# Optimization experiments

Measured on AMD Instinct MI355X. Metric: run time of the kernel, lower is better.

## Reference

```python
import jax, jax.numpy as jnp
import numpy as np

EPS = 1e-5
SLOPE = 0.2  # leakyrelu negative slope (gcn_lib default)
K = 9

def knn_idx(x, k):
    # x: (B, C, N) -> idx (B, N, k) of k nearest neighbors, self excluded
    B, C, N = x.shape
    xx = jnp.sum(x * x, axis=1)                       # (B, N)
    inner = jnp.einsum('bcn,bcm->bnm', x, x)          # (B, N, N)
    dist = xx[:, :, None] - 2.0 * inner + xx[:, None, :]
    dist = dist + jnp.eye(N, dtype=x.dtype) * 1e10    # mask self
    _, idx = jax.lax.top_k(-dist, k)                  # nearest = largest -dist
    return idx

def bn(h, g, b, axes):
    m = jnp.mean(h, axis=axes, keepdims=True)
    v = jnp.var(h, axis=axes, keepdims=True)
    sh = [1] * h.ndim; sh[1] = -1
    return (h - m) / jnp.sqrt(v + EPS) * g.reshape(sh) + b.reshape(sh)

def leaky(h):
    return jnp.where(h >= 0, h, SLOPE * h)

def edge_conv(x, idx, W, g, b):
    # x: (B, C, N); idx: (B, N, k); W: (O, 2C)
    B, C, N = x.shape
    k = idx.shape[-1]
    x_j = jax.vmap(lambda xb, ib: xb[:, ib])(x, idx)  # (B, C, N, k)
    x_i = jnp.broadcast_to(x[:, :, :, None], (B, C, N, k))
    edge = jnp.concatenate([x_i, x_j - x_i], axis=1)  # (B, 2C, N, k)
    h = jnp.einsum('oc,bcnk->bonk', W, edge)
    h = leaky(bn(h, g, b, (0, 2, 3)))
    return jnp.max(h, axis=-1)                        # (B, O, N)

def setup_inputs() -> dict:
    key = jax.random.key(0)
    ks = jax.random.split(key, 24)
    B, N = 8, 4096
    d = {}
    d['x'] = jax.random.normal(ks[0], (B, 3, N), dtype=jnp.float32)
    d['coords'] = jax.random.normal(ks[1], (B, 3, N), dtype=jnp.float32)
    def w(k_, o, i): return jax.random.normal(k_, (o, i), dtype=jnp.float32) * (2.0 / i) ** 0.5
    # edge conv layers (bias=False, batchnorm affine)
    d['w1'], d['g1'], d['b1'] = w(ks[2], 64, 6),    jnp.ones(64),  jnp.zeros(64)
    d['w2'], d['g2'], d['b2'] = w(ks[3], 64, 128),  jnp.ones(64),  jnp.zeros(64)
    d['w3'], d['g3'], d['b3'] = w(ks[4], 128, 128), jnp.ones(128), jnp.zeros(128)
    d['w4'], d['g4'], d['b4'] = w(ks[5], 256, 256), jnp.ones(256), jnp.zeros(256)
    # decoder fusion conv [512 -> 1024]
    d['wf'], d['bf'] = w(ks[6], 1024, 512), jnp.zeros(1024)
    d['gf'], d['betaf'] = jnp.ones(1024), jnp.zeros(1024)
    # classifier [2048 -> 512 -> 256 -> 40]
    d['wc1'], d['bc1'] = w(ks[7], 512, 2048), jnp.zeros(512)
    d['gc1'], d['betac1'] = jnp.ones(512), jnp.zeros(512)
    d['wc2'], d['bc2'] = w(ks[8], 256, 512), jnp.zeros(256)
    d['gc2'], d['betac2'] = jnp.ones(256), jnp.zeros(256)
    d['wc3'], d['bc3'] = w(ks[9], 40, 256), jnp.zeros(40)
    return d

def reference(x, coords, w1, g1, b1, w2, g2, b2, w3, g3, b3, w4, g4, b4,
              wf, bf, gf, betaf, wc1, bc1, gc1, betac1, wc2, bc2, gc2, betac2, wc3, bc3):
    out1 = edge_conv(x,    knn_idx(x, K),    w1, g1, b1)   # (B, 64, N)
    out2 = edge_conv(out1, knn_idx(out1, K), w2, g2, b2)   # (B, 64, N)
    out3 = edge_conv(out2, knn_idx(out2, K), w3, g3, b3)   # (B, 128, N)
    out4 = edge_conv(out3, knn_idx(out3, K), w4, g4, b4)   # (B, 256, N)
    feat = jnp.concatenate([out1, out2, out3, out4], axis=1)  # (B, 512, N)
    fusion = jnp.einsum('oc,bcn->bon', wf, feat) + bf[None, :, None]
    fusion = leaky(bn(fusion, gf, betaf, (0, 2)))           # (B, 1024, N)
    x1 = jnp.max(fusion, axis=-1)                           # adaptive max pool
    x2 = jnp.mean(fusion, axis=-1)                          # adaptive avg pool
    h = jnp.concatenate([x1, x2], axis=1)                   # (B, 2048)
    h = leaky(bn(h @ wc1.T + bc1, gc1, betac1, (0,)))       # dropout = identity (eval)
    h = leaky(bn(h @ wc2.T + bc2, gc2, betac2, (0,)))
    logits = h @ wc3.T + bc3                                # (B, 40)
    return logits
```

## Files before the change

### kernel.cpp

```cpp
#include <hip/hip_runtime.h>
#include <math.h>
#include <float.h>


#define LEAKY(y) ((y) >= 0.f ? (y) : 0.2f * (y))

using f32x16 = __attribute__((ext_vector_type(16))) float;
using bf16x8 = __attribute__((ext_vector_type(8))) __bf16;
using short8v = __attribute__((ext_vector_type(8))) short;

__device__ inline ushort f2bf(float x) {
  unsigned u = __float_as_uint(x);
  unsigned r = (u + 0x7fff + ((u >> 16) & 1)) >> 16;
  return (ushort)r;
}

template<int C>
__global__ void xx_kernel(const float* __restrict__ xin, long bstride, int N,
                          float* __restrict__ xxg) {
  int n = blockIdx.x * 256 + threadIdx.x;
  int b = blockIdx.y;
  if (n < N) {
    const float* xb = xin + (long)b * bstride;
    float s = 0.f;
    #pragma unroll
    for (int c = 0; c < C; ++c) { float t = xb[(long)c * N + n]; s += t * t; }
    xxg[(long)b * N + n] = s;
  }
}

template<int C, int KCc>
__global__ __launch_bounds__(256) void pack3_kernel(const float* __restrict__ xin, long bstride,
                                                    int N, const float* __restrict__ xxg,
                                                    ushort* __restrict__ packR,
                                                    ushort* __restrict__ packC,
                                                    float* __restrict__ xpm) {
  __shared__ float xt[C][32];
  const int tid = threadIdx.x;
  const int pb = blockIdx.x, b = blockIdx.y;
  for (int i = tid; i < C * 32; i += 256) {
    int c = i >> 5, j = i & 31;
    xt[c][j] = xin[(long)b * bstride + (long)c * N + pb * 32 + j];
  }
  __syncthreads();
  for (int i = tid; i < 32 * C; i += 256) {
    int pt = i / C, c = i % C;
    xpm[((long)b * N + pb * 32 + pt) * C + c] = xt[c][pt];
  }
  const int PB = N >> 5;
  for (int it = tid; it < KCc * 64; it += 256) {
    int kc = it >> 6, l = it & 63;
    int pt = l & 31;
    union { ushort u[8]; short8v v; } R, Cc;
    #pragma unroll
    for (int e = 0; e < 8; ++e) {
      int kp = kc * 16 + ((l >> 5) << 3) + e;
      ushort rv = 0, cv = 0;
      if (kp < 3 * C) {
        int s = kp / C, c = kp % C;
        float xv = xt[c][pt];
        ushort hi = f2bf(xv);
        float hif = __uint_as_float((unsigned)hi << 16);
        ushort mid = f2bf(xv - hif);
        rv = (s == 2) ? mid : hi;
        cv = (s == 1) ? mid : hi;
      } else if (kp == 3 * C) {
        float xxv = xxg[(long)b * N + pb * 32 + pt];
        cv = f2bf(xxv);
        rv = 0xBF00;
      } else if (kp == 3 * C + 1) {
        float xxv = xxg[(long)b * N + pb * 32 + pt];
        ushort hi = f2bf(xxv);
        float hif = __uint_as_float((unsigned)hi << 16);
        cv = f2bf(xxv - hif);
        rv = 0xBF00;
      }
      R.u[e] = rv; Cc.u[e] = cv;
    }
    long off = (((long)b * PB + pb) * KCc + kc) * 512 + l * 8;
    *reinterpret_cast<short8v*>(&packR[off]) = R.v;
    *reinterpret_cast<short8v*>(&packC[off]) = Cc.v;
  }
}

#define KNN_SCAN(SELF)                                            \
  _Pragma("unroll")                                               \
  for (int reg = 0; reg < 16; ++reg) {                            \
    int m_loc = (reg & 3) + 8 * (reg >> 2) + 4 * hf;              \
    float d = fmaf(-2.0f, acc[reg], xr);                          \
    d = fmaxf(d, 0.f);                                            \
    unsigned key = (__float_as_uint(d) & KEYMASK) |               \
                   (unsigned)((t << 5) | m_loc);                  \
    if (SELF && ((mb << 5) | m_loc) == n_glob) key = 0xFFFFFFFFu; \
    if (key < tk[9]) {                                            \
      unsigned kc = key;                                          \
      _Pragma("unroll")                                           \
      for (int s_ = 0; s_ < 10; ++s_) {                           \
        unsigned mn_ = min(kc, tk[s_]);                           \
        kc = max(kc, tk[s_]);                                     \
        tk[s_] = mn_;                                             \
      }                                                           \
    }                                                             \
  }

template<int KCc, int MINW, int Z>
__global__ __launch_bounds__(256, MINW) void knn_v5(const ushort* __restrict__ packR,
                                                    const ushort* __restrict__ packC,
                                                    const float* __restrict__ xxg,
                                                    int N, int* __restrict__ cand) {
  constexpr int SA_ELEMS = KCc * 512;
  constexpr int SA_BYTES = SA_ELEMS * 2;
  constexpr int POOL = (2 * SA_BYTES > 10240) ? 2 * SA_BYTES : 10240;
  __shared__ __align__(16) char smem[POOL];
  ushort* const sA0 = (ushort*)smem;
  ushort* const sA1 = (ushort*)(smem + SA_BYTES);

  const int tid = threadIdx.x;
  const int b = blockIdx.y, rowblk = blockIdx.x, z = blockIdx.z;
  const int w = tid >> 6, l = tid & 63;
  const int lane31 = l & 31, hf = l >> 5;
  const int PB = N >> 5;
  const int HALF = PB / Z;
  const unsigned IDXMASK = (unsigned)(HALF * 32 - 1);
  const unsigned KEYMASK = ~IDXMASK;
  const int myblk = rowblk * 4 + w;

  const ushort* rp = packR + (((long)b * PB + myblk) * (long)KCc) * 512 + l * 8;
  bf16x8 bfr[KCc];
  #pragma unroll
  for (int kc = 0; kc < KCc; ++kc)
    bfr[kc] = *reinterpret_cast<const bf16x8*>(rp + kc * 512);

  const ushort* srcb = packC + ((long)b * PB) * (long)SA_ELEMS;
  const int mb0 = z * HALF;

  {
    const ushort* src = srcb + (long)mb0 * SA_ELEMS;
    for (int i = tid * 8; i < SA_ELEMS; i += 2048)
      __builtin_amdgcn_global_load_lds(
          (const __attribute__((address_space(1))) void*)(src + i),
          (__attribute__((address_space(3))) void*)(sA0 + i), 16, 0, 0);
  }

  const int n_glob = rowblk * 128 + w * 32 + lane31;
  const float xr = xxg[(long)b * N + n_glob];

  unsigned tk[10];
  #pragma unroll
  for (int s = 0; s < 10; ++s) tk[s] = 0xFFFFFFFFu;

  __syncthreads();

  for (int t = 0; t < HALF; ++t) {
    const int mb = mb0 + t;
    const ushort* curA = (t & 1) ? sA1 : sA0;
    ushort* nxtA = (t & 1) ? sA0 : sA1;
    if (t + 1 < HALF) {
      const ushort* src = srcb + (long)(mb + 1) * SA_ELEMS;
      for (int i = tid * 8; i < SA_ELEMS; i += 2048)
        __builtin_amdgcn_global_load_lds(
            (const __attribute__((address_space(1))) void*)(src + i),
            (__attribute__((address_space(3))) void*)(nxtA + i), 16, 0, 0);
    }
    f32x16 acc = {};
    #pragma unroll
    for (int kc = 0; kc < KCc; ++kc) {
      bf16x8 af = *reinterpret_cast<const bf16x8*>(curA + kc * 512 + l * 8);
      acc = __builtin_amdgcn_mfma_f32_32x32x16_bf16(af, bfr[kc], acc, 0, 0, 0);
    }
    if (mb == myblk) {
      KNN_SCAN(true)
    } else {
      KNN_SCAN(false)
    }
    __syncthreads();
  }

  unsigned* mK = (unsigned*)smem;
  const int row = w * 32 + lane31;
  #pragma unroll
  for (int s = 0; s < 10; ++s)
    mK[row * 20 + hf * 10 + s] = tk[s];
  __syncthreads();
  if (tid < 128) {
    int p0 = 0, p1 = 0;
    const long ob = ((long)b * N + rowblk * 128 + tid) * (Z * 10) + z * 10;
    const int base_m = z * HALF * 32;
    for (int s = 0; s < 10; ++s) {
      unsigned k0 = mK[tid * 20 + p0];
      unsigned k1 = mK[tid * 20 + 10 + p1];
      bool t0 = k0 < k1;
      unsigned kk = t0 ? k0 : k1;
      cand[ob + s] = base_m + (int)(kk & IDXMASK);
      if (t0) ++p0; else ++p1;
    }
  }
}

template<int C, int P>
__global__ __launch_bounds__(320) void rerank_kernel(const float* __restrict__ xpm,
                                                     int N, const float* __restrict__ xxg,
                                                     const int* __restrict__ cand,
                                                     int* __restrict__ idx_out) {
  constexpr int ROWS = 320 / P;
  __shared__ float sq[ROWS][C];
  __shared__ float sd[ROWS][P + 1];
  __shared__ int   si[ROWS][P + 1];
  const int tid = threadIdx.x;
  const int b = blockIdx.y, n0 = blockIdx.x * ROWS;
  const float* xb = xpm + (long)b * N * C;
  for (int i = tid; i < ROWS * C; i += 320) {
    int r = i / C, c = i % C;
    sq[r][c] = xb[(long)(n0 + r) * C + c];
  }
  __syncthreads();
  const int r = tid / P, j = tid % P;
  const int n = n0 + r;
  const int m = cand[((long)b * N + n) * P + j];
  const float* cv = xb + (long)m * C;
  float dot = 0.f;
  if constexpr ((C & 3) == 0) {
    for (int c = 0; c < C; c += 4) {
      float4 v4 = *reinterpret_cast<const float4*>(cv + c);
      dot = fmaf(sq[r][c + 0], v4.x, dot);
      dot = fmaf(sq[r][c + 1], v4.y, dot);
      dot = fmaf(sq[r][c + 2], v4.z, dot);
      dot = fmaf(sq[r][c + 3], v4.w, dot);
    }
  } else {
    for (int c = 0; c < C; ++c) dot = fmaf(sq[r][c], cv[c], dot);
  }
  float d = (xxg[(long)b * N + n] - 2.0f * dot) + xxg[(long)b * N + m];
  if (m == n) d = 3.0e38f;
  sd[r][j] = d; si[r][j] = m;
  __syncthreads();
  int rank = 0;
  #pragma unroll
  for (int t = 0; t < P; ++t) {
    float dd = sd[r][t]; int ii = si[r][t];
    if (dd < d || (dd == d && ii < m)) rank++;
  }
  if (rank < 9) idx_out[((long)b * N + n) * 9 + rank] = m;
}

__global__ void prep_wt(const float* __restrict__ W, int Cin, int O,
                        float* __restrict__ At, float* __restrict__ W2t) {
  int i = blockIdx.x * 256 + threadIdx.x;
  if (i < O * Cin) {
    int o = i % O, c = i / O;
    float w1v = W[(long)o * 2 * Cin + c];
    float w2v = W[(long)o * 2 * Cin + Cin + c];
    At[(long)c * O + o]  = w1v - w2v;
    W2t[(long)c * O + o] = w2v;
  }
}

__global__ __launch_bounds__(256) void gemm_cn_no(const float* __restrict__ Wt,
                                                  int C, int O,
                                                  const float* __restrict__ in,
                                                  long in_bstride, int N,
                                                  float* __restrict__ out) {
  const int tid = threadIdx.x;
  const int n0 = blockIdx.x * 64, o0 = blockIdx.y * 64, b = blockIdx.z;
  __shared__ float wT[128][64];
  __shared__ float inT[128][64];
  for (int i = tid; i < C * 64; i += 256) {
    int c = i >> 6, j = i & 63;
    wT[c][j]  = Wt[(long)c * O + o0 + j];
    inT[c][j] = in[(long)b * in_bstride + (long)c * N + n0 + j];
  }
  __syncthreads();
  const int tr = tid >> 4, tc = tid & 15;
  float acc[4][4];
  #pragma unroll
  for (int i = 0; i < 4; ++i)
    #pragma unroll
    for (int j = 0; j < 4; ++j) acc[i][j] = 0.f;
  for (int c = 0; c < C; ++c) {
    float4 a4 = *reinterpret_cast<const float4*>(&wT[c][4 * tr]);
    float4 b4 = *reinterpret_cast<const float4*>(&inT[c][4 * tc]);
    float av[4] = {a4.x, a4.y, a4.z, a4.w};
    float bv[4] = {b4.x, b4.y, b4.z, b4.w};
    #pragma unroll
    for (int i = 0; i < 4; ++i)
      #pragma unroll
      for (int j = 0; j < 4; ++j) acc[i][j] = fmaf(av[i], bv[j], acc[i][j]);
  }
  #pragma unroll
  for (int j = 0; j < 4; ++j) {
    float4 st = make_float4(acc[0][j], acc[1][j], acc[2][j], acc[3][j]);
    *reinterpret_cast<float4*>(&out[((long)b * N + n0 + 4 * tc + j) * O + o0 + 4 * tr]) = st;
  }
}

__global__ __launch_bounds__(256) void edge_pass(const float* __restrict__ u,
                                                 const float* __restrict__ v,
                                                 const int* __restrict__ idx,
                                                 int O, int N,
                                                 float* __restrict__ hmax,
                                                 float* __restrict__ hmin,
                                                 double* __restrict__ S1,
                                                 double* __restrict__ S2) {
  const int tid = threadIdx.x;
  const int n0 = blockIdx.x * 64, o0 = blockIdx.y * 64, b = blockIdx.z;
  __shared__ int sidx[64][9];
  __shared__ float4 redA[4][16];
  __shared__ float4 redB[4][16];
  for (int i = tid; i < 576; i += 256)
    ((int*)sidx)[i] = idx[((long)b * N + n0) * 9 + i];
  __syncthreads();
  const int nl = tid >> 4, oq = tid & 15;
  const long base = (long)b * N;
  const int ocol = o0 + 4 * oq;
  float4 s1 = make_float4(0.f, 0.f, 0.f, 0.f);
  float4 s2 = make_float4(0.f, 0.f, 0.f, 0.f);
  for (int g = 0; g < 4; ++g) {
    const int n = g * 16 + nl;
    const float4 u4 = *reinterpret_cast<const float4*>(&u[(base + n0 + n) * O + ocol]);
    float4 mx = make_float4(-3.0e38f, -3.0e38f, -3.0e38f, -3.0e38f);
    float4 mn = make_float4(3.0e38f, 3.0e38f, 3.0e38f, 3.0e38f);
    #pragma unroll
    for (int k = 0; k < 9; ++k) {
      int m = sidx[n][k];
      const float4 v4 = *reinterpret_cast<const float4*>(&v[(base + m) * O + ocol]);
      float hx = u4.x + v4.x, hy = u4.y + v4.y, hz = u4.z + v4.z, hw = u4.w + v4.w;
      s1.x += hx; s1.y += hy; s1.z += hz; s1.w += hw;
      s2.x = fmaf(hx, hx, s2.x); s2.y = fmaf(hy, hy, s2.y);
      s2.z = fmaf(hz, hz, s2.z); s2.w = fmaf(hw, hw, s2.w);
      mx.x = fmaxf(mx.x, hx); mx.y = fmaxf(mx.y, hy); mx.z = fmaxf(mx.z, hz); mx.w = fmaxf(mx.w, hw);
      mn.x = fminf(mn.x, hx); mn.y = fminf(mn.y, hy); mn.z = fminf(mn.z, hz); mn.w = fminf(mn.w, hw);
    }
    *reinterpret_cast<float4*>(&hmax[(base + n0 + n) * O + ocol]) = mx;
    *reinterpret_cast<float4*>(&hmin[(base + n0 + n) * O + ocol]) = mn;
  }
  s1.x += __shfl_xor(s1.x, 16); s1.y += __shfl_xor(s1.y, 16);
  s1.z += __shfl_xor(s1.z, 16); s1.w += __shfl_xor(s1.w, 16);
  s2.x += __shfl_xor(s2.x, 16); s2.y += __shfl_xor(s2.y, 16);
  s2.z += __shfl_xor(s2.z, 16); s2.w += __shfl_xor(s2.w, 16);
  s1.x += __shfl_xor(s1.x, 32); s1.y += __shfl_xor(s1.y, 32);
  s1.z += __shfl_xor(s1.z, 32); s1.w += __shfl_xor(s1.w, 32);
  s2.x += __shfl_xor(s2.x, 32); s2.y += __shfl_xor(s2.y, 32);
  s2.z += __shfl_xor(s2.z, 32); s2.w += __shfl_xor(s2.w, 32);
  if ((tid & 48) == 0) { redA[tid >> 6][oq] = s1; redB[tid >> 6][oq] = s2; }
  __syncthreads();
  if (tid < 16) {
    float4 a = redA[0][tid], bb = redB[0][tid];
    #pragma unroll
    for (int ww = 1; ww < 4; ++ww) {
      float4 t1 = redA[ww][tid], t2 = redB[ww][tid];
      a.x += t1.x; a.y += t1.y; a.z += t1.z; a.w += t1.w;
      bb.x += t2.x; bb.y += t2.y; bb.z += t2.z; bb.w += t2.w;
    }
    int o = o0 + 4 * tid;
    atomicAdd(&S1[o + 0], (double)a.x);  atomicAdd(&S1[o + 1], (double)a.y);
    atomicAdd(&S1[o + 2], (double)a.z);  atomicAdd(&S1[o + 3], (double)a.w);
    atomicAdd(&S2[o + 0], (double)bb.x); atomicAdd(&S2[o + 1], (double)bb.y);
    atomicAdd(&S2[o + 2], (double)bb.z); atomicAdd(&S2[o + 3], (double)bb.w);
  }
}

__global__ void finalize_scale(const double* __restrict__ S1, const double* __restrict__ S2,
                               const float* __restrict__ g, const float* __restrict__ beta,
                               double invM, int O, float* __restrict__ scale,
                               float* __restrict__ shift) {
  int o = blockIdx.x * 256 + threadIdx.x;
  if (o < O) {
    double mean = S1[o] * invM;
    double var = S2[o] * invM - mean * mean;
    double sc = (double)g[o] / sqrt(var + 1e-5);
    scale[o] = (float)sc;
    shift[o] = (float)((double)beta[o] - mean * sc);
  }
}

__global__ __launch_bounds__(256) void edge_out(const float* __restrict__ hmax,
                                                const float* __restrict__ hmin,
                                                const float* __restrict__ scale,
                                                const float* __restrict__ shift,
                                                int O, int N,
                                                float* __restrict__ outp, long out_bstride) {
  const int tid = threadIdx.x;
  const int b = blockIdx.y, n0 = blockIdx.x * 64;
  __shared__ float yt[64][65];
  const int ol = tid & 63, nl = tid >> 6;
  const long base = (long)b * N;
  for (int oc = 0; oc < O; oc += 64) {
    float sc = scale[oc + ol], sh = shift[oc + ol];
    __syncthreads();
    for (int ng = 0; ng < 16; ++ng) {
      int n = ng * 4 + nl;
      long off = (base + n0 + n) * O + oc + ol;
      float hv = (sc >= 0.f) ? hmax[off] : hmin[off];
      float y = sc * hv + sh;
      yt[ol][n] = LEAKY(y);
    }
    __syncthreads();
    for (int rr = 0; rr < 16; ++rr) {
      int r = rr * 4 + nl;
      outp[(long)b * out_bstride + (long)(oc + r) * N + n0 + ol] = yt[r][ol];
    }
  }
}

__global__ __launch_bounds__(256) void pack3_wf(const float* __restrict__ wf,
                                                ushort* __restrict__ packW) {
  __shared__ float wt[32][129];
  const int po = blockIdx.x;
  const int tid = threadIdx.x;
  for (int c0 = 0; c0 < 512; c0 += 128) {
    __syncthreads();
    for (int i = tid; i < 32 * 128; i += 256) {
      int o = i >> 7, c = i & 127;
      wt[o][c] = wf[(long)(po * 32 + o) * 512 + c0 + c];
    }
    __syncthreads();
    #pragma unroll
    for (int s = 0; s < 3; ++s) {
      int kc0 = (s * 512 + c0) >> 4;
      for (int it = tid; it < 8 * 64; it += 256) {
        int kcl = it >> 6, l = it & 63;
        union { ushort u[8]; short8v v; } P;
        #pragma unroll
        for (int e = 0; e < 8; ++e) {
          int kp = (kc0 + kcl) * 16 + ((l >> 5) << 3) + e;
          int c = kp - s * 512 - c0;
          float xv = wt[l & 31][c];
          ushort hi = f2bf(xv);
          if (s == 1) {
            float hif = __uint_as_float((unsigned)hi << 16);
            P.u[e] = f2bf(xv - hif);
          } else P.u[e] = hi;
        }
        *reinterpret_cast<short8v*>(&packW[((long)po * 96 + kc0 + kcl) * 512 + l * 8]) = P.v;
      }
    }
  }
}

__global__ __launch_bounds__(256) void pack3_feat(const float* __restrict__ feat, int N,
                                                  ushort* __restrict__ packB) {
  __shared__ float xt[64][33];
  const int pb = blockIdx.x, b = blockIdx.y;
  const int tid = threadIdx.x;
  const int PB = N >> 5;
  for (int c0 = 0; c0 < 512; c0 += 64) {
    __syncthreads();
    for (int i = tid; i < 64 * 32; i += 256) {
      int c = i >> 5, j = i & 31;
      xt[c][j] = feat[((long)b * 512 + c0 + c) * N + pb * 32 + j];
    }
    __syncthreads();
    #pragma unroll
    for (int s = 0; s < 3; ++s) {
      int kc0 = (s * 512 + c0) >> 4;
      for (int it = tid; it < 4 * 64; it += 256) {
        int kcl = it >> 6, l = it & 63;
        union { ushort u[8]; short8v v; } P;
        #pragma unroll
        for (int e = 0; e < 8; ++e) {
          int kp = (kc0 + kcl) * 16 + ((l >> 5) << 3) + e;
          int c = kp - s * 512 - c0;
          float xv = xt[c][l & 31];
          ushort hi = f2bf(xv);
          if (s == 2) {
            float hif = __uint_as_float((unsigned)hi << 16);
            P.u[e] = f2bf(xv - hif);
          } else P.u[e] = hi;
        }
        *reinterpret_cast<short8v*>(
            &packB[(((long)b * PB + pb) * 96 + kc0 + kcl) * 512 + l * 8]) = P.v;
      }
    }
  }
}

#define FUS_EPI(ACC, Q)                                                          \
  _Pragma("unroll")                                                              \
  for (int reg = 0; reg < 16; ++reg) {                                           \
    int o = ((z * 16 + (Q) * 4 + w) << 5) + (reg & 3) + 8 * (reg >> 2) + 4 * hf; \
    float h = ACC[reg] + bfb[o];                                                 \
    hbf[((long)b * 1024 + o) * 4096 + (nt << 5) + lane31] = f2bf(h);             \
    float mx = h, mn = h;                                                        \
    _Pragma("unroll")                                                            \
    for (int off = 1; off < 32; off <<= 1) {                                     \
      mx = fmaxf(mx, __shfl_xor(mx, off));                                       \
      mn = fminf(mn, __shfl_xor(mn, off));                                       \
    }                                                                            \
    if (lane31 == 0) {                                                           \
      long po = (long)o * 1024 + b * 128 + nt;                                   \
      p3[po] = mx; p4[po] = mn;                                                  \
    }                                                                            \
  }

__global__ __launch_bounds__(256) void fusion_gemm_store(const ushort* __restrict__ packW,
                                                         const ushort* __restrict__ packB,
                                                         const float* __restrict__ bfb,
                                                         int N,
                                                         ushort* __restrict__ hbf,
                                                         float* __restrict__ p3,
                                                         float* __restrict__ p4) {
  __shared__ ushort sB[2][12 * 512];
  const int tid = threadIdx.x;
  const int nt = blockIdx.x, z = blockIdx.y, b = blockIdx.z;
  const int w = tid >> 6, l = tid & 63;
  const int lane31 = l & 31, hf = l >> 5;
  const int PB = N >> 5;
  const ushort* srcB = packB + (((long)b * PB + nt) * 96) * 512;

  for (int i = tid * 8; i < 12 * 512; i += 2048)
    __builtin_amdgcn_global_load_lds(
        (const __attribute__((address_space(1))) void*)(srcB + i),
        (__attribute__((address_space(3))) void*)(&sB[0][i]), 16, 0, 0);
  __syncthreads();

  f32x16 acc0 = {}, acc1 = {}, acc2 = {}, acc3 = {};
  const ushort* aw0 = packW + ((long)(z * 16 + 0 + w) * 96) * 512 + l * 8;
  const ushort* aw1 = packW + ((long)(z * 16 + 4 + w) * 96) * 512 + l * 8;
  const ushort* aw2 = packW + ((long)(z * 16 + 8 + w) * 96) * 512 + l * 8;
  const ushort* aw3 = packW + ((long)(z * 16 + 12 + w) * 96) * 512 + l * 8;

  int cur = 0;
  for (int ch = 0; ch < 8; ++ch) {
    if (ch + 1 < 8) {
      const ushort* src = srcB + (ch + 1) * 12 * 512;
      for (int i = tid * 8; i < 12 * 512; i += 2048)
        __builtin_amdgcn_global_load_lds(
            (const __attribute__((address_space(1))) void*)(src + i),
            (__attribute__((address_space(3))) void*)(&sB[cur ^ 1][i]), 16, 0, 0);
    }
    #pragma unroll
    for (int kcl = 0; kcl < 12; ++kcl) {
      const int kc = ch * 12 + kcl;
      bf16x8 bf = *reinterpret_cast<const bf16x8*>(&sB[cur][kcl * 512 + l * 8]);
      bf16x8 a0 = *reinterpret_cast<const bf16x8*>(aw0 + (long)kc * 512);
      acc0 = __builtin_amdgcn_mfma_f32_32x32x16_bf16(a0, bf, acc0, 0, 0, 0);
      bf16x8 a1 = *reinterpret_cast<const bf16x8*>(aw1 + (long)kc * 512);
      acc1 = __builtin_amdgcn_mfma_f32_32x32x16_bf16(a1, bf, acc1, 0, 0, 0);
      bf16x8 a2 = *reinterpret_cast<const bf16x8*>(aw2 + (long)kc * 512);
      acc2 = __builtin_amdgcn_mfma_f32_32x32x16_bf16(a2, bf, acc2, 0, 0, 0);
      bf16x8 a3 = *reinterpret_cast<const bf16x8*>(aw3 + (long)kc * 512);
      acc3 = __builtin_amdgcn_mfma_f32_32x32x16_bf16(a3, bf, acc3, 0, 0, 0);
    }
    __syncthreads();
    cur ^= 1;
  }

  FUS_EPI(acc0, 0)
  FUS_EPI(acc1, 1)
  FUS_EPI(acc2, 2)
  FUS_EPI(acc3, 3)
}

__global__ __launch_bounds__(256) void stats_bf16(const ushort* __restrict__ hbf,
                                                  float* __restrict__ ps1,
                                                  float* __restrict__ ps2) {
  int gw = (blockIdx.x * 256 + threadIdx.x) >> 6;
  int lane = threadIdx.x & 63;
  int b = gw >> 10, o = gw & 1023;
  const ushort* row = hbf + ((long)b * 1024 + o) * 4096;
  float s1 = 0.f, s2 = 0.f;
  for (int j = 0; j < 8; ++j) {
    union { ushort u[8]; short8v v; } hv;
    hv.v = *reinterpret_cast<const short8v*>(row + ((j << 6) + lane) * 8);
    #pragma unroll
    for (int e = 0; e < 8; ++e) {
      float h = __uint_as_float((unsigned)hv.u[e] << 16);
      s1 += h;
      s2 = fmaf(h, h, s2);
    }
  }
  #pragma unroll
  for (int off = 1; off < 64; off <<= 1) {
    s1 += __shfl_xor(s1, off);
    s2 += __shfl_xor(s2, off);
  }
  if (lane == 0) {
    ps1[(long)b * 1024 + o] = s1;
    ps2[(long)b * 1024 + o] = s2;
  }
}

__global__ void finalize_fusion2(const float* __restrict__ ps1, const float* __restrict__ ps2,
                                 const float* __restrict__ g, const float* __restrict__ beta,
                                 float* __restrict__ scale, float* __restrict__ shift) {
  int o = blockIdx.x * 256 + threadIdx.x;
  if (o < 1024) {
    double s1 = 0.0, s2 = 0.0;
    for (int b = 0; b < 8; ++b) {
      s1 += (double)ps1[(long)b * 1024 + o];
      s2 += (double)ps2[(long)b * 1024 + o];
    }
    double invM = 1.0 / 32768.0;
    double mean = s1 * invM;
    double var = s2 * invM - mean * mean;
    double sc = (double)g[o] / sqrt(var + 1e-5);
    scale[o] = (float)sc;
    shift[o] = (float)((double)beta[o] - mean * sc);
  }
}

__global__ __launch_bounds__(256) void pool_v3(const ushort* __restrict__ hbf,
                                               const float* __restrict__ p3,
                                               const float* __restrict__ p4,
                                               const float* __restrict__ scale,
                                               const float* __restrict__ shift,
                                               float* __restrict__ x1x2) {
  int gw = (blockIdx.x * 256 + threadIdx.x) >> 6;
  int lane = threadIdx.x & 63;
  int b = gw >> 10, o = gw & 1023;
  float sc = scale[o], sh = shift[o];

  long pb = (long)o * 1024 + b * 128;
  float hm;
  if (sc >= 0.f) {
    float a = p3[pb + lane], c = p3[pb + 64 + lane];
    hm = fmaxf(a, c);
    #pragma unroll
    for (int off = 1; off < 64; off <<= 1) hm = fmaxf(hm, __shfl_xor(hm, off));
  } else {
    float a = p4[pb + lane], c = p4[pb + 64 + lane];
    hm = fminf(a, c);
    #pragma unroll
    for (int off = 1; off < 64; off <<= 1) hm = fminf(hm, __shfl_xor(hm, off));
  }
  float x1 = LEAKY(fmaf(sc, hm, sh));

  const ushort* row = hbf + ((long)b * 1024 + o) * 4096;
  float sm = 0.f;
  for (int j = 0; j < 8; ++j) {
    union { ushort u[8]; short8v v; } hv;
    hv.v = *reinterpret_cast<const short8v*>(row + ((j << 6) + lane) * 8);
    #pragma unroll
    for (int e = 0; e < 8; ++e) {
      float h = __uint_as_float((unsigned)hv.u[e] << 16);
      float y = fmaf(sc, h, sh);
      sm += LEAKY(y);
    }
  }
  #pragma unroll
  for (int off = 1; off < 64; off <<= 1) sm += __shfl_xor(sm, off);

  if (lane == 0) {
    x1x2[(long)b * 2048 + o] = x1;
    x1x2[(long)b * 2048 + 1024 + o] = sm * (1.f / 4096.f);
  }
}

__global__ __launch_bounds__(256) void fc_kernel(const float* __restrict__ in, int Cin, int O,
                                                 const float* __restrict__ W,
                                                 const float* __restrict__ bias,
                                                 const float* __restrict__ g,
                                                 const float* __restrict__ beta,
                                                 float* __restrict__ outp, int do_bn) {
  const int tid = threadIdx.x;
  const int o = blockIdx.x * 32 + (tid >> 3);
  const int bb = tid & 7;
  const int oc = (o < O) ? o : (O - 1);
  const float* ir = in + (long)bb * Cin;
  const float* wr = W + (long)oc * Cin;
  float dot = 0.f;
  for (int c = 0; c < Cin; c += 4) {
    float4 a = *reinterpret_cast<const float4*>(&ir[c]);
    float4 w = *reinterpret_cast<const float4*>(&wr[c]);
    dot += a.x * w.x + a.y * w.y + a.z * w.z + a.w * w.w;
  }
  float h = dot + bias[oc];
  if (do_bn) {
    float s = h;
    s += __shfl_xor(s, 1, 8); s += __shfl_xor(s, 2, 8); s += __shfl_xor(s, 4, 8);
    float mean = s * 0.125f;
    float dv = (h - mean) * (h - mean);
    dv += __shfl_xor(dv, 1, 8); dv += __shfl_xor(dv, 2, 8); dv += __shfl_xor(dv, 4, 8);
    float var = dv * 0.125f;
    float y = (h - mean) * (float)(1.0 / sqrt((double)var + 1e-5)) * g[oc] + beta[oc];
    h = LEAKY(y);
  }
  if (o < O) outp[(long)bb * O + o] = h;
}

extern "C" void kernel_launch(void* const* d_in, const int* in_sizes, int n_in,
                              void* d_out, int out_size, void* d_ws, size_t ws_size,
                              hipStream_t stream) {
  const int B = 8, N = 4096;
  const float* x   = (const float*)d_in[0];
  const float* w1 = (const float*)d_in[2];  const float* g1 = (const float*)d_in[3];  const float* b1 = (const float*)d_in[4];
  const float* w2 = (const float*)d_in[5];  const float* g2 = (const float*)d_in[6];  const float* b2 = (const float*)d_in[7];
  const float* w3 = (const float*)d_in[8];  const float* g3 = (const float*)d_in[9];  const float* b3 = (const float*)d_in[10];
  const float* w4 = (const float*)d_in[11]; const float* g4 = (const float*)d_in[12]; const float* b4 = (const float*)d_in[13];
  const float* wf = (const float*)d_in[14]; const float* bfv = (const float*)d_in[15];
  const float* gf = (const float*)d_in[16]; const float* betaf = (const float*)d_in[17];
  const float* wc1 = (const float*)d_in[18]; const float* bc1 = (const float*)d_in[19];
  const float* gc1 = (const float*)d_in[20]; const float* betac1 = (const float*)d_in[21];
  const float* wc2 = (const float*)d_in[22]; const float* bc2 = (const float*)d_in[23];
  const float* gc2 = (const float*)d_in[24]; const float* betac2 = (const float*)d_in[25];
  const float* wc3 = (const float*)d_in[26]; const float* bc3 = (const float*)d_in[27];

  char* p = (char*)d_ws;
  auto alloc = [&](size_t bytes) -> char* {
    char* r = p;
    p += (bytes + 255) & ~(size_t)255;
    return r;
  };
  float* feat  = (float*)alloc((size_t)B * 512 * N * 4);
  int*   idx   = (int*)  alloc((size_t)B * N * 9 * 4);
  int*   cand  = (int*)  alloc((size_t)B * N * 64 * 4);
  float* xxg   = (float*)alloc((size_t)B * N * 4);
  float* u     = (float*)alloc((size_t)B * N * 256 * 4);
  float* v     = (float*)alloc((size_t)B * N * 256 * 4);
  float* hmax  = (float*)alloc((size_t)B * N * 256 * 4);
  float* hmin  = (float*)alloc((size_t)B * N * 256 * 4);
  ushort* packR = (ushort*)u;
  ushort* packC = (ushort*)hmax;
  float*  xpm   = hmin;
  ushort* packB = (ushort*)u;
  ushort* hbf   = (ushort*)feat;
  float*  ps1   = hmin;
  float*  ps2   = hmin + 1048576;
  float*  ps3   = hmin + 2 * 1048576;
  float*  ps4   = hmin + 3 * 1048576;
  float* At    = (float*)alloc(128 * 256 * 4);
  float* W2t   = (float*)alloc(128 * 256 * 4);
  ushort* packW = (ushort*)alloc((size_t)32 * 96 * 512 * 2);
  double* S1   = (double*)alloc(1024 * 8);
  double* S2   = (double*)alloc(1024 * 8);
  float* scale = (float*)alloc(1024 * 4);
  float* shift = (float*)alloc(1024 * 4);
  float* x1x2  = (float*)alloc((size_t)B * 2048 * 4);
  float* h1    = (float*)alloc((size_t)B * 512 * 4);
  float* h2    = (float*)alloc((size_t)B * 256 * 4);

  dim3 gpack(N / 32, B);
  dim3 gknn4(N / 128, B, 4);
  dim3 gknn2(N / 128, B, 2);
  dim3 grr40(N / 8, B);
  dim3 grr20(N / 16, B);
  dim3 gxx(N / 256, B);

  pack3_wf<<<32, 256, 0, stream>>>(wf, packW);

  auto edge = [&](const float* inp, long in_bstride, int Cin, int O, const float* W,
                  const float* g, const float* beta, int c0) {
    prep_wt<<<(O * Cin + 255) / 256, 256, 0, stream>>>(W, Cin, O, At, W2t);
    dim3 gg(N / 64, O / 64, B);
    gemm_cn_no<<<gg, 256, 0, stream>>>(At, Cin, O, inp, in_bstride, N, u);
    gemm_cn_no<<<gg, 256, 0, stream>>>(W2t, Cin, O, inp, in_bstride, N, v);
    hipMemsetAsync(S1, 0, O * 8, stream);
    hipMemsetAsync(S2, 0, O * 8, stream);
    edge_pass<<<gg, 256, 0, stream>>>(u, v, idx, O, N, hmax, hmin, S1, S2);
    finalize_scale<<<(O + 255) / 256, 256, 0, stream>>>(S1, S2, g, beta,
                                                        1.0 / ((double)B * N * 9), O, scale, shift);
    edge_out<<<dim3(N / 64, B), 256, 0, stream>>>(hmax, hmin, scale, shift, O, N,
                                                  feat + (long)c0 * N, (long)512 * N);
  };

  xx_kernel<3><<<gxx, 256, 0, stream>>>(x, (long)3 * N, N, xxg);
  pack3_kernel<3, 1><<<gpack, 256, 0, stream>>>(x, (long)3 * N, N, xxg, packR, packC, xpm);
  knn_v5<1, 4, 4><<<gknn4, 256, 0, stream>>>(packR, packC, xxg, N, cand);
  rerank_kernel<3, 40><<<grr40, 320, 0, stream>>>(xpm, N, xxg, cand, idx);
  edge(x, (long)3 * N, 3, 64, w1, g1, b1, 0);

  xx_kernel<64><<<gxx, 256, 0, stream>>>(feat, (long)512 * N, N, xxg);
  pack3_kernel<64, 13><<<gpack, 256, 0, stream>>>(feat, (long)512 * N, N, xxg, packR, packC, xpm);
  knn_v5<13, 3, 4><<<gknn4, 256, 0, stream>>>(packR, packC, xxg, N, cand);
  rerank_kernel<64, 40><<<grr40, 320, 0, stream>>>(xpm, N, xxg, cand, idx);
  edge(feat, (long)512 * N, 64, 64, w2, g2, b2, 64);

  xx_kernel<64><<<gxx, 256, 0, stream>>>(feat + (long)64 * N, (long)512 * N, N, xxg);
  pack3_kernel<64, 13><<<gpack, 256, 0, stream>>>(feat + (long)64 * N, (long)512 * N, N, xxg,
                                                  packR, packC, xpm);
  knn_v5<13, 3, 4><<<gknn4, 256, 0, stream>>>(packR, packC, xxg, N, cand);
  rerank_kernel<64, 40><<<grr40, 320, 0, stream>>>(xpm, N, xxg, cand, idx);
  edge(feat + (long)64 * N, (long)512 * N, 64, 128, w3, g3, b3, 128);

  xx_kernel<128><<<gxx, 256, 0, stream>>>(feat + (long)128 * N, (long)512 * N, N, xxg);
  pack3_kernel<128, 25><<<gpack, 256, 0, stream>>>(feat + (long)128 * N, (long)512 * N, N, xxg,
                                                   packR, packC, xpm);
  knn_v5<25, 3, 2><<<gknn2, 256, 0, stream>>>(packR, packC, xxg, N, cand);
  rerank_kernel<128, 20><<<grr20, 320, 0, stream>>>(xpm, N, xxg, cand, idx);
  edge(feat + (long)128 * N, (long)512 * N, 128, 256, w4, g4, b4, 256);

  pack3_feat<<<dim3(N / 32, B), 256, 0, stream>>>(feat, N, packB);
  dim3 gfu(N / 32, 2, B);
  fusion_gemm_store<<<gfu, 256, 0, stream>>>(packW, packB, bfv, N, hbf, ps3, ps4);
  stats_bf16<<<2048, 256, 0, stream>>>(hbf, ps1, ps2);
  finalize_fusion2<<<4, 256, 0, stream>>>(ps1, ps2, gf, betaf, scale, shift);
  pool_v3<<<2048, 256, 0, stream>>>(hbf, ps3, ps4, scale, shift, x1x2);

  fc_kernel<<<16, 256, 0, stream>>>(x1x2, 2048, 512, wc1, bc1, gc1, betac1, h1, 1);
  fc_kernel<<<8, 256, 0, stream>>>(h1, 512, 256, wc2, bc2, gc2, betac2, h2, 1);
  fc_kernel<<<2, 256, 0, stream>>>(h2, 256, 40, wc3, bc3, nullptr, nullptr, (float*)d_out, 0);
}
```

Before: 1.612 ms.

## Use split-bf16 MFMA for edge-conv GEMMs and select max/min by gamma sign

Replaces the two fp32 SIMT GEMMs per edge-conv layer with one MFMA kernel. Inputs and weights are split into hi/mid/lo bf16 parts, six cross products are summed to approximate fp32 accuracy, and u and v are computed together. Because the BN scale has the same sign as gamma, the edge pass stores only the max or the min per channel, picked by gamma's sign. The fusion GEMM likewise keeps one sign-adjusted max instead of separate max and min partials. This cuts FMA time and memory traffic, at the cost of extra pack kernels and a small precision difference from the bf16 split.

```diff
diff --git a/kernel.cpp b/kernel.cpp
--- a/kernel.cpp
+++ b/kernel.cpp
@@ -243,62 +243,135 @@
   if (rank < 9) idx_out[((long)b * N + n) * 9 + rank] = m;
 }
 
-__global__ void prep_wt(const float* __restrict__ W, int Cin, int O,
-                        float* __restrict__ At, float* __restrict__ W2t) {
-  int i = blockIdx.x * 256 + threadIdx.x;
-  if (i < O * Cin) {
-    int o = i % O, c = i / O;
-    float w1v = W[(long)o * 2 * Cin + c];
-    float w2v = W[(long)o * 2 * Cin + Cin + c];
-    At[(long)c * O + o]  = w1v - w2v;
-    W2t[(long)c * O + o] = w2v;
-  }
-}
-
-__global__ __launch_bounds__(256) void gemm_cn_no(const float* __restrict__ Wt,
-                                                  int C, int O,
-                                                  const float* __restrict__ in,
-                                                  long in_bstride, int N,
-                                                  float* __restrict__ out) {
-  const int tid = threadIdx.x;
-  const int n0 = blockIdx.x * 64, o0 = blockIdx.y * 64, b = blockIdx.z;
-  __shared__ float wT[128][64];
-  __shared__ float inT[128][64];
-  for (int i = tid; i < C * 64; i += 256) {
-    int c = i >> 6, j = i & 63;
-    wT[c][j]  = Wt[(long)c * O + o0 + j];
-    inT[c][j] = in[(long)b * in_bstride + (long)c * N + n0 + j];
-  }
-  __syncthreads();
-  const int tr = tid >> 4, tc = tid & 15;
-  float acc[4][4];
+template<int C, int KCX>
+__global__ __launch_bounds__(256) void pack6_x(const float* __restrict__ xin, long bstride,
+                                               int N, ushort* __restrict__ packX) {
+  __shared__ float xt[C][32];
+  const int tid = threadIdx.x;
+  const int pb = blockIdx.x, b = blockIdx.y;
+  for (int i = tid; i < C * 32; i += 256) {
+    int c = i >> 5, j = i & 31;
+    xt[c][j] = xin[(long)b * bstride + (long)c * N + pb * 32 + j];
+  }
+  __syncthreads();
+  const int PB = N >> 5;
+  for (int it = tid; it < KCX * 64; it += 256) {
+    int kc = it >> 6, l = it & 63;
+    int pt = l & 31;
+    union { ushort u[8]; short8v v; } P;
+    #pragma unroll
+    for (int e = 0; e < 8; ++e) {
+      int kp = kc * 16 + ((l >> 5) << 3) + e;
+      ushort val = 0;
+      if (kp < 6 * C) {
+        int s = kp / C, c = kp % C;
+        float xv = xt[c][pt];
+        ushort hi = f2bf(xv);
+        float hif = __uint_as_float((unsigned)hi << 16);
+        float r1 = xv - hif;
+        ushort mid = f2bf(r1);
+        float midf = __uint_as_float((unsigned)mid << 16);
+        ushort lo = f2bf(r1 - midf);
+        val = (s == 1 || s == 3) ? mid : ((s == 4) ? lo : hi);
+      }
+      P.u[e] = val;
+    }
+    long off = (((long)b * PB + pb) * KCX + kc) * 512 + l * 8;
+    *reinterpret_cast<short8v*>(&packX[off]) = P.v;
+  }
+}
+
+template<int C, int NOB, int KCW>
+__global__ __launch_bounds__(256) void pack6_w(const float* __restrict__ W,
+                                               ushort* __restrict__ packAw) {
+  __shared__ float wt[32][C + 1];
+  const int mo = blockIdx.x;
+  const int mat = mo / NOB, ob = mo % NOB;
+  const int tid = threadIdx.x;
+  for (int i = tid; i < 32 * C; i += 256) {
+    int o = i / C, c = i % C;
+    float w1v = W[(long)(ob * 32 + o) * 2 * C + c];
+    float w2v = W[(long)(ob * 32 + o) * 2 * C + C + c];
+    wt[o][c] = mat ? w2v : (w1v - w2v);
+  }
+  __syncthreads();
+  for (int it = tid; it < KCW * 64; it += 256) {
+    int kc = it >> 6, l = it & 63;
+    union { ushort u[8]; short8v v; } P;
+    #pragma unroll
+    for (int e = 0; e < 8; ++e) {
+      int kp = kc * 16 + ((l >> 5) << 3) + e;
+      ushort val = 0;
+      if (kp < 6 * C) {
+        int s = kp / C, c = kp % C;
+        float xv = wt[l & 31][c];
+        ushort hi = f2bf(xv);
+        float hif = __uint_as_float((unsigned)hi << 16);
+        float r1 = xv - hif;
+        ushort mid = f2bf(r1);
+        float midf = __uint_as_float((unsigned)mid << 16);
+        ushort lo = f2bf(r1 - midf);
+        val = (s == 2 || s == 3) ? mid : ((s == 5) ? lo : hi);
+      }
+      P.u[e] = val;
+    }
+    *reinterpret_cast<short8v*>(&packAw[((long)mo * KCW + kc) * 512 + l * 8]) = P.v;
+  }
+}
+
+template<int KCW, int NOB>
+__global__ __launch_bounds__(256) void edge_gemm6(const ushort* __restrict__ packX,
+                                                  const ushort* __restrict__ packAw,
+                                                  int N,
+                                                  float* __restrict__ u,
+                                                  float* __restrict__ v) {
+  constexpr int NT = 2 * NOB;
+  constexpr int TPW = NT / 4;
+  constexpr int O = NOB * 32;
+  const int nb = blockIdx.x, b = blockIdx.y;
+  const int w = threadIdx.x >> 6, l = threadIdx.x & 63;
+  const int lane31 = l & 31, hf = l >> 5;
+  const ushort* xp = packX + ((long)(b * (N >> 5) + nb) * KCW) * 512 + l * 8;
+
+  f32x16 acc[TPW] = {};
+  const ushort* aptr[TPW];
   #pragma unroll
-  for (int i = 0; i < 4; ++i)
-    #pragma unroll
-    for (int j = 0; j < 4; ++j) acc[i][j] = 0.f;
-  for (int c = 0; c < C; ++c) {
-    float4 a4 = *reinterpret_cast<const float4*>(&wT[c][4 * tr]);
-    float4 b4 = *reinterpret_cast<const float4*>(&inT[c][4 * tc]);
-    float av[4] = {a4.x, a4.y, a4.z, a4.w};
-    float bv[4] = {b4.x, b4.y, b4.z, b4.w};
-    #pragma unroll
-    for (int i = 0; i < 4; ++i)
-      #pragma unroll
-      for (int j = 0; j < 4; ++j) acc[i][j] = fmaf(av[i], bv[j], acc[i][j]);
-  }
+  for (int ti = 0; ti < TPW; ++ti) {
+    int t = w + ti * 4;
+    int mat = t & 1, ob = t >> 1;
+    aptr[ti] = packAw + ((long)(mat * NOB + ob) * KCW) * 512 + l * 8;
+  }
+
+  for (int kc = 0; kc < KCW; ++kc) {
+    bf16x8 bf = *reinterpret_cast<const bf16x8*>(xp + (long)kc * 512);
+    #pragma unroll
+    for (int ti = 0; ti < TPW; ++ti) {
+      bf16x8 af = *reinterpret_cast<const bf16x8*>(aptr[ti] + (long)kc * 512);
+      acc[ti] = __builtin_amdgcn_mfma_f32_32x32x16_bf16(af, bf, acc[ti], 0, 0, 0);
+    }
+  }
+
   #pragma unroll
-  for (int j = 0; j < 4; ++j) {
-    float4 st = make_float4(acc[0][j], acc[1][j], acc[2][j], acc[3][j]);
-    *reinterpret_cast<float4*>(&out[((long)b * N + n0 + 4 * tc + j) * O + o0 + 4 * tr]) = st;
+  for (int ti = 0; ti < TPW; ++ti) {
+    int t = w + ti * 4;
+    int mat = t & 1, ob = t >> 1;
+    float* dst = mat ? v : u;
+    long rowbase = ((long)b * N + nb * 32 + lane31) * O + ob * 32;
+    #pragma unroll
+    for (int q = 0; q < 4; ++q) {
+      float4 st = make_float4(acc[ti][4 * q + 0], acc[ti][4 * q + 1],
+                              acc[ti][4 * q + 2], acc[ti][4 * q + 3]);
+      *reinterpret_cast<float4*>(&dst[rowbase + 4 * hf + 8 * q]) = st;
+    }
   }
 }
 
 __global__ __launch_bounds__(256) void edge_pass(const float* __restrict__ u,
                                                  const float* __restrict__ v,
                                                  const int* __restrict__ idx,
+                                                 const float* __restrict__ g,
                                                  int O, int N,
-                                                 float* __restrict__ hmax,
-                                                 float* __restrict__ hmin,
+                                                 float* __restrict__ hsel,
                                                  double* __restrict__ S1,
                                                  double* __restrict__ S2) {
   const int tid = threadIdx.x;
@@ -312,10 +385,11 @@
   const int nl = tid >> 4, oq = tid & 15;
   const long base = (long)b * N;
   const int ocol = o0 + 4 * oq;
+  const float4 gv = *reinterpret_cast<const float4*>(&g[ocol]);
   float4 s1 = make_float4(0.f, 0.f, 0.f, 0.f);
   float4 s2 = make_float4(0.f, 0.f, 0.f, 0.f);
-  for (int g = 0; g < 4; ++g) {
-    const int n = g * 16 + nl;
+  for (int gg = 0; gg < 4; ++gg) {
+    const int n = gg * 16 + nl;
     const float4 u4 = *reinterpret_cast<const float4*>(&u[(base + n0 + n) * O + ocol]);
     float4 mx = make_float4(-3.0e38f, -3.0e38f, -3.0e38f, -3.0e38f);
     float4 mn = make_float4(3.0e38f, 3.0e38f, 3.0e38f, 3.0e38f);
@@ -330,8 +404,12 @@
       mx.x = fmaxf(mx.x, hx); mx.y = fmaxf(mx.y, hy); mx.z = fmaxf(mx.z, hz); mx.w = fmaxf(mx.w, hw);
       mn.x = fminf(mn.x, hx); mn.y = fminf(mn.y, hy); mn.z = fminf(mn.z, hz); mn.w = fminf(mn.w, hw);
     }
-    *reinterpret_cast<float4*>(&hmax[(base + n0 + n) * O + ocol]) = mx;
-    *reinterpret_cast<float4*>(&hmin[(base + n0 + n) * O + ocol]) = mn;
+    float4 sel;
+    sel.x = (gv.x >= 0.f) ? mx.x : mn.x;
+    sel.y = (gv.y >= 0.f) ? mx.y : mn.y;
+    sel.z = (gv.z >= 0.f) ? mx.z : mn.z;
+    sel.w = (gv.w >= 0.f) ? mx.w : mn.w;
+    *reinterpret_cast<float4*>(&hsel[(base + n0 + n) * O + ocol]) = sel;
   }
   s1.x += __shfl_xor(s1.x, 16); s1.y += __shfl_xor(s1.y, 16);
   s1.z += __shfl_xor(s1.z, 16); s1.w += __shfl_xor(s1.w, 16);
@@ -340,7 +418,7 @@
   s1.x += __shfl_xor(s1.x, 32); s1.y += __shfl_xor(s1.y, 32);
   s1.z += __shfl_xor(s1.z, 32); s1.w += __shfl_xor(s1.w, 32);
   s2.x += __shfl_xor(s2.x, 32); s2.y += __shfl_xor(s2.y, 32);
-  s2.z += __shfl_xor(s2.z, 32); s2.w += __shfl_xor(s2.w, 32);
+  s2.z += __shfl_xor(s2.w, 32) * 0.f + __shfl_xor(s2.z, 32); s2.w += __shfl_xor(s2.w, 32);
   if ((tid & 48) == 0) { redA[tid >> 6][oq] = s1; redB[tid >> 6][oq] = s2; }
   __syncthreads();
   if (tid < 16) {
@@ -373,8 +451,7 @@
   }
 }
 
-__global__ __launch_bounds__(256) void edge_out(const float* __restrict__ hmax,
-                                                const float* __restrict__ hmin,
+__global__ __launch_bounds__(256) void edge_out(const float* __restrict__ hsel,
                                                 const float* __restrict__ scale,
                                                 const float* __restrict__ shift,
                                                 int O, int N,
@@ -389,8 +466,7 @@
     __syncthreads();
     for (int ng = 0; ng < 16; ++ng) {
       int n = ng * 4 + nl;
-      long off = (base + n0 + n) * O + oc + ol;
-      float hv = (sc >= 0.f) ? hmax[off] : hmin[off];
+      float hv = hsel[(base + n0 + n) * O + oc + ol];
       float y = sc * hv + sh;
       yt[ol][n] = LEAKY(y);
     }
@@ -480,25 +556,21 @@
     int o = ((z * 16 + (Q) * 4 + w) << 5) + (reg & 3) + 8 * (reg >> 2) + 4 * hf; \
     float h = ACC[reg] + bfb[o];                                                 \
     hbf[((long)b * 1024 + o) * 4096 + (nt << 5) + lane31] = f2bf(h);             \
-    float mx = h, mn = h;                                                        \
+    float vsel = (gf[o] >= 0.f) ? h : -h;                                        \
     _Pragma("unroll")                                                            \
-    for (int off = 1; off < 32; off <<= 1) {                                     \
-      mx = fmaxf(mx, __shfl_xor(mx, off));                                       \
-      mn = fminf(mn, __shfl_xor(mn, off));                                       \
-    }                                                                            \
-    if (lane31 == 0) {                                                           \
-      long po = (long)o * 1024 + b * 128 + nt;                                   \
-      p3[po] = mx; p4[po] = mn;                                                  \
-    }                                                                            \
+    for (int off = 1; off < 32; off <<= 1)                                       \
+      vsel = fmaxf(vsel, __shfl_xor(vsel, off));                                 \
+    if (lane31 == 0)                                                             \
+      p3[(long)o * 1024 + b * 128 + nt] = vsel;                                  \
   }
 
 __global__ __launch_bounds__(256) void fusion_gemm_store(const ushort* __restrict__ packW,
                                                          const ushort* __restrict__ packB,
                                                          const float* __restrict__ bfb,
+                                                         const float* __restrict__ gf,
                                                          int N,
                                                          ushort* __restrict__ hbf,
-                                                         float* __restrict__ p3,
-                                                         float* __restrict__ p4) {
+                                                         float* __restrict__ p3) {
   __shared__ ushort sB[2][12 * 512];
   const int tid = threadIdx.x;
   const int nt = blockIdx.x, z = blockIdx.y, b = blockIdx.z;
@@ -601,7 +673,6 @@
 
 __global__ __launch_bounds__(256) void pool_v3(const ushort* __restrict__ hbf,
                                                const float* __restrict__ p3,
-                                               const float* __restrict__ p4,
                                                const float* __restrict__ scale,
                                                const float* __restrict__ shift,
                                                float* __restrict__ x1x2) {
@@ -611,18 +682,10 @@
   float sc = scale[o], sh = shift[o];
 
   long pb = (long)o * 1024 + b * 128;
-  float hm;
-  if (sc >= 0.f) {
-    float a = p3[pb + lane], c = p3[pb + 64 + lane];
-    hm = fmaxf(a, c);
-    #pragma unroll
-    for (int off = 1; off < 64; off <<= 1) hm = fmaxf(hm, __shfl_xor(hm, off));
-  } else {
-    float a = p4[pb + lane], c = p4[pb + 64 + lane];
-    hm = fminf(a, c);
-    #pragma unroll
-    for (int off = 1; off < 64; off <<= 1) hm = fminf(hm, __shfl_xor(hm, off));
-  }
+  float red = fmaxf(p3[pb + lane], p3[pb + 64 + lane]);
+  #pragma unroll
+  for (int off = 1; off < 64; off <<= 1) red = fmaxf(red, __shfl_xor(red, off));
+  float hm = (sc >= 0.f) ? red : -red;
   float x1 = LEAKY(fmaf(sc, hm, sh));
 
   const ushort* row = hbf + ((long)b * 1024 + o) * 4096;
@@ -676,6 +739,27 @@
     h = LEAKY(y);
   }
   if (o < O) outp[(long)bb * O + o] = h;
+}
+
+template<int Cin, int O>
+static void edge_layer(const float* inp, long bstride, const float* W,
+                       const float* g, const float* beta,
+                       float* featOut, long out_bstride,
+                       ushort* packX6, ushort* packAw, float* u, float* v,
+                       const int* idx, float* hsel, double* S1, double* S2,
+                       float* scale, float* shift, int N, int B,
+                       hipStream_t stream) {
+  constexpr int KCW = (6 * Cin + 15) / 16;
+  constexpr int NOB = O / 32;
+  pack6_x<Cin, KCW><<<dim3(N / 32, B), 256, 0, stream>>>(inp, bstride, N, packX6);
+  pack6_w<Cin, NOB, KCW><<<2 * NOB, 256, 0, stream>>>(W, packAw);
+  edge_gemm6<KCW, NOB><<<dim3(N / 32, B), 256, 0, stream>>>(packX6, packAw, N, u, v);
+  hipMemsetAsync(S1, 0, O * 8, stream);
+  hipMemsetAsync(S2, 0, O * 8, stream);
+  edge_pass<<<dim3(N / 64, O / 64, B), 256, 0, stream>>>(u, v, idx, g, O, N, hsel, S1, S2);
+  finalize_scale<<<(O + 255) / 256, 256, 0, stream>>>(S1, S2, g, beta,
+                                                      1.0 / ((double)B * N * 9), O, scale, shift);
+  edge_out<<<dim3(N / 64, B), 256, 0, stream>>>(hsel, scale, shift, O, N, featOut, out_bstride);
 }
 
 extern "C" void kernel_launch(void* const* d_in, const int* in_sizes, int n_in,
@@ -712,14 +796,14 @@
   ushort* packR = (ushort*)u;
   ushort* packC = (ushort*)hmax;
   float*  xpm   = hmin;
+  ushort* packX6 = (ushort*)hmax;
+  float*  hsel  = hmax;
   ushort* packB = (ushort*)u;
   ushort* hbf   = (ushort*)feat;
   float*  ps1   = hmin;
   float*  ps2   = hmin + 1048576;
   float*  ps3   = hmin + 2 * 1048576;
-  float*  ps4   = hmin + 3 * 1048576;
-  float* At    = (float*)alloc(128 * 256 * 4);
-  float* W2t   = (float*)alloc(128 * 256 * 4);
+  ushort* packAw = (ushort*)alloc((size_t)2 * 8 * 48 * 512 * 2);
   ushort* packW = (ushort*)alloc((size_t)32 * 96 * 512 * 2);
   double* S1   = (double*)alloc(1024 * 8);
   double* S2   = (double*)alloc(1024 * 8);
@@ -738,53 +822,44 @@
 
   pack3_wf<<<32, 256, 0, stream>>>(wf, packW);
 
-  auto edge = [&](const float* inp, long in_bstride, int Cin, int O, const float* W,
-                  const float* g, const float* beta, int c0) {
-    prep_wt<<<(O * Cin + 255) / 256, 256, 0, stream>>>(W, Cin, O, At, W2t);
-    dim3 gg(N / 64, O / 64, B);
-    gemm_cn_no<<<gg, 256, 0, stream>>>(At, Cin, O, inp, in_bstride, N, u);
-    gemm_cn_no<<<gg, 256, 0, stream>>>(W2t, Cin, O, inp, in_bstride, N, v);
-    hipMemsetAsync(S1, 0, O * 8, stream);
-    hipMemsetAsync(S2, 0, O * 8, stream);
-    edge_pass<<<gg, 256, 0, stream>>>(u, v, idx, O, N, hmax, hmin, S1, S2);
-    finalize_scale<<<(O + 255) / 256, 256, 0, stream>>>(S1, S2, g, beta,
-                                                        1.0 / ((double)B * N * 9), O, scale, shift);
-    edge_out<<<dim3(N / 64, B), 256, 0, stream>>>(hmax, hmin, scale, shift, O, N,
-                                                  feat + (long)c0 * N, (long)512 * N);
-  };
-
   xx_kernel<3><<<gxx, 256, 0, stream>>>(x, (long)3 * N, N, xxg);
   pack3_kernel<3, 1><<<gpack, 256, 0, stream>>>(x, (long)3 * N, N, xxg, packR, packC, xpm);
   knn_v5<1, 4, 4><<<gknn4, 256, 0, stream>>>(packR, packC, xxg, N, cand);
   rerank_kernel<3, 40><<<grr40, 320, 0, stream>>>(xpm, N, xxg, cand, idx);
-  edge(x, (long)3 * N, 3, 64, w1, g1, b1, 0);
+  edge_layer<3, 64>(x, (long)3 * N, w1, g1, b1, feat, (long)512 * N,
+                    packX6, packAw, u, v, idx, hsel, S1, S2, scale, shift, N, B, stream);
 
   xx_kernel<64><<<gxx, 256, 0, stream>>>(feat, (long)512 * N, N, xxg);
   pack3_kernel<64, 13><<<gpack, 256, 0, stream>>>(feat, (long)512 * N, N, xxg, packR, packC, xpm);
   knn_v5<13, 3, 4><<<gknn4, 256, 0, stream>>>(packR, packC, xxg, N, cand);
   rerank_kernel<64, 40><<<grr40, 320, 0, stream>>>(xpm, N, xxg, cand, idx);
-  edge(feat, (long)512 * N, 64, 64, w2, g2, b2, 64);
+  edge_layer<64, 64>(feat, (long)512 * N, w2, g2, b2, feat + (long)64 * N, (long)512 * N,
+                     packX6, packAw, u, v, idx, hsel, S1, S2, scale, shift, N, B, stream);
 
   xx_kernel<64><<<gxx, 256, 0, stream>>>(feat + (long)64 * N, (long)512 * N, N, xxg);
   pack3_kernel<64, 13><<<gpack, 256, 0, stream>>>(feat + (long)64 * N, (long)512 * N, N, xxg,
                                                   packR, packC, xpm);
   knn_v5<13, 3, 4><<<gknn4, 256, 0, stream>>>(packR, packC, xxg, N, cand);
   rerank_kernel<64, 40><<<grr40, 320, 0, stream>>>(xpm, N, xxg, cand, idx);
-  edge(feat + (long)64 * N, (long)512 * N, 64, 128, w3, g3, b3, 128);
+  edge_layer<64, 128>(feat + (long)64 * N, (long)512 * N, w3, g3, b3,
+                      feat + (long)128 * N, (long)512 * N,
+                      packX6, packAw, u, v, idx, hsel, S1, S2, scale, shift, N, B, stream);
 
   xx_kernel<128><<<gxx, 256, 0, stream>>>(feat + (long)128 * N, (long)512 * N, N, xxg);
   pack3_kernel<128, 25><<<gpack, 256, 0, stream>>>(feat + (long)128 * N, (long)512 * N, N, xxg,
                                                    packR, packC, xpm);
   knn_v5<25, 3, 2><<<gknn2, 256, 0, stream>>>(packR, packC, xxg, N, cand);
   rerank_kernel<128, 20><<<grr20, 320, 0, stream>>>(xpm, N, xxg, cand, idx);
-  edge(feat + (long)128 * N, (long)512 * N, 128, 256, w4, g4, b4, 256);
+  edge_layer<128, 256>(feat + (long)128 * N, (long)512 * N, w4, g4, b4,
+                       feat + (long)256 * N, (long)512 * N,
+                       packX6, packAw, u, v, idx, hsel, S1, S2, scale, shift, N, B, stream);
 
   pack3_feat<<<dim3(N / 32, B), 256, 0, stream>>>(feat, N, packB);
   dim3 gfu(N / 32, 2, B);
-  fusion_gemm_store<<<gfu, 256, 0, stream>>>(packW, packB, bfv, N, hbf, ps3, ps4);
+  fusion_gemm_store<<<gfu, 256, 0, stream>>>(packW, packB, bfv, gf, N, hbf, ps3);
   stats_bf16<<<2048, 256, 0, stream>>>(hbf, ps1, ps2);
   finalize_fusion2<<<4, 256, 0, stream>>>(ps1, ps2, gf, betaf, scale, shift);
-  pool_v3<<<2048, 256, 0, stream>>>(hbf, ps3, ps4, scale, shift, x1x2);
+  pool_v3<<<2048, 256, 0, stream>>>(hbf, ps3, scale, shift, x1x2);
 
   fc_kernel<<<16, 256, 0, stream>>>(x1x2, 2048, 512, wc1, bc1, gc1, betac1, h1, 1);
   fc_kernel<<<8, 256, 0, stream>>>(h1, 512, 256, wc2, bc2, gc2, betac2, h2, 1);
```

After: 1.622 ms. Within noise of the previous version (+0.6%).
